# Performance work log

Measured on AMD Instinct MI355X. Metric: run time of the kernel, lower is better.

## Reference

```python
import jax, jax.numpy as jnp
import numpy as np

DIM_EMB = 1024
NUM_HEADS = 16
DIM_HEAD = DIM_EMB // NUM_HEADS  # 64


def setup_inputs() -> dict:
    key = jax.random.key(0)
    k1, k2, k3 = jax.random.split(key, 3)
    x = jax.random.normal(k1, (4, 2048, DIM_EMB), dtype=jnp.float32)
    # nn.Linear(dim_embedding, 3*h*d, bias=False): weight shape [out, in]
    w_qkv = jax.random.normal(k2, (3 * NUM_HEADS * DIM_HEAD, DIM_EMB), dtype=jnp.float32) * (DIM_EMB ** -0.5)
    w_out = jax.random.normal(k3, (DIM_EMB, NUM_HEADS * DIM_HEAD), dtype=jnp.float32) * ((NUM_HEADS * DIM_HEAD) ** -0.5)
    return {"x": x, "w_qkv": w_qkv, "w_out": w_out}


def reference(x, w_qkv, w_out):
    b, t, _ = x.shape
    scale = DIM_HEAD ** -0.5
    qkv = jnp.einsum('bte,fe->btf', x, w_qkv)  # [b, t, 3*h*d]
    qkv = qkv.reshape(b, t, 3, NUM_HEADS, DIM_HEAD)  # fused dim order (k h d)
    q, k, v = qkv[:, :, 0], qkv[:, :, 1], qkv[:, :, 2]  # each [b, t, h, d]
    scores = jnp.einsum('bihd,bjhd->bhij', q, k) * scale  # [b, h, t, t]
    weights = jax.nn.softmax(scores, axis=-1)
    attn = jnp.einsum('bhij,bjhd->bhid', weights, v)  # [b, h, t, d]
    concat = attn.transpose(0, 2, 1, 3).reshape(b, t, NUM_HEADS * DIM_HEAD)
    return jnp.einsum('btf,ef->bte', concat, w_out)
```

## Files before the change

### kernel.cpp

```cpp
#include <hip/hip_runtime.h>

#define DI __device__ __forceinline__

typedef float  f32x2  __attribute__((ext_vector_type(2)));
typedef float  f32x4  __attribute__((ext_vector_type(4)));
typedef float  f32x16 __attribute__((ext_vector_type(16)));
typedef __bf16 bf16x8 __attribute__((ext_vector_type(8)));
typedef unsigned u32x2 __attribute__((ext_vector_type(2)));
typedef unsigned u32x4 __attribute__((ext_vector_type(4)));

static constexpr int TB   = 2048;
static constexpr int NTOK = 8192;
static constexpr int EMB  = 1024;
static constexpr int FQKV = 3072;

DI unsigned short f2bf(float f) {
  union { float f; unsigned u; } v; v.f = f;
  unsigned r = v.u + 0x7FFFu + ((v.u >> 16) & 1u);
  return (unsigned short)(r >> 16);
}

DI unsigned pack2bf(float a, float b) {
#if __has_builtin(__builtin_amdgcn_cvt_pk_bf16_f32)
  typedef __bf16 bf16x2 __attribute__((ext_vector_type(2)));
  bf16x2 r = __builtin_amdgcn_cvt_pk_bf16_f32(a, b);
  return __builtin_bit_cast(unsigned, r);
#else
  unsigned ua = __builtin_bit_cast(unsigned, a) + 0x8000u;
  unsigned ub = __builtin_bit_cast(unsigned, b) + 0x8000u;
  return __builtin_amdgcn_perm(ub, ua, 0x07060302u);
#endif
}

DI void plswap(unsigned& a, unsigned& b) {
#if __has_builtin(__builtin_amdgcn_permlane32_swap)
  u32x2 r = __builtin_amdgcn_permlane32_swap(a, b, false, false);
  a = r.x; b = r.y;
#else
  const bool hi = (threadIdx.x & 32) != 0;
  unsigned ax = (unsigned)__shfl_xor((int)a, 32);
  unsigned bx = (unsigned)__shfl_xor((int)b, 32);
  unsigned na = hi ? bx : a;
  unsigned nb = hi ? b : ax;
  a = na; b = nb;
#endif
}

DI bf16x8 frag4(unsigned a, unsigned b, unsigned c, unsigned d) {
  u32x4 u = {a, b, c, d};
  return __builtin_bit_cast(bf16x8, u);
}

DI void gload16(const void* g, void* l) {
  __builtin_amdgcn_global_load_lds(
      (__attribute__((address_space(1))) void*)(g),
      (__attribute__((address_space(3))) void*)(l), 16, 0, 0);
}

DI void wait_vm8() { asm volatile("s_waitcnt vmcnt(8)" ::: "memory"); }
DI void wait_vm4() { asm volatile("s_waitcnt vmcnt(4)" ::: "memory"); }
DI void wait_vm0() { asm volatile("s_waitcnt vmcnt(0)" ::: "memory"); }
DI void rbar()     { __builtin_amdgcn_s_barrier(); }
DI void sfence()   { __builtin_amdgcn_sched_barrier(0); }

__global__ __launch_bounds__(256)
void cvt_kernel(const float4* __restrict__ x, const float4* __restrict__ wq,
                const float4* __restrict__ wo,
                ushort4* __restrict__ xb, ushort4* __restrict__ wqb,
                ushort4* __restrict__ wob) {
  const int i  = blockIdx.x * 256 + threadIdx.x;
  const int nx = NTOK * EMB / 4;
  const int nq = FQKV * EMB / 4;
  float4 v; ushort4* dst;
  if (i < nx)           { v = x[i];           dst = xb  + i; }
  else if (i < nx + nq) { v = wq[i - nx];     dst = wqb + (i - nx); }
  else                  { v = wo[i - nx - nq]; dst = wob + (i - nx - nq); }
  ushort4 p;
  p.x = f2bf(v.x); p.y = f2bf(v.y); p.z = f2bf(v.z); p.w = f2bf(v.w);
  *dst = p;
}

__global__ __launch_bounds__(512, 2)
void gemm256(const unsigned short* __restrict__ A,
             const unsigned short* __restrict__ Bt,
             const int K,
             unsigned short* __restrict__ qk,
             unsigned short* __restrict__ vT) {
  __shared__ unsigned short sA[2][256 * 64];
  __shared__ unsigned short sB[2][256 * 64];
  const int tid  = threadIdx.x;
  const int w    = tid >> 6;
  const int l    = tid & 63;
  const int quad = l >> 4;
  const int lr   = l & 15;
  const int nwg  = gridDim.x * gridDim.y;
  const int orig = blockIdx.y * gridDim.x + blockIdx.x;
  const int swz  = (orig & 7) * (nwg >> 3) + (orig >> 3);
  const int n0   = (swz % gridDim.x) * 256;
  const int m0   = (swz / gridDim.x) * 256;
  const int wm   = (w >> 2) * 128;
  const int wn   = (w & 3) * 64;

  f32x4 acc[8][4];
#pragma unroll
  for (int i = 0; i < 8; ++i)
#pragma unroll
    for (int j = 0; j < 4; ++j) acc[i][j] = {0.f, 0.f, 0.f, 0.f};

  const int srow8 = l >> 3;
  const int gsw   = ((l & 7) ^ srow8) * 8;
  const unsigned short* gA0 = A  + (long)(m0 + w * 8 + srow8) * K + gsw;
  const unsigned short* gB0 = Bt + (long)(n0 + w * 8 + srow8) * K + gsw;

  const int NT = K >> 6;

#define STAGE256(buf, kk)                                                      \
  do {                                                                         \
    _Pragma("unroll")                                                          \
    for (int jj = 0; jj < 4; ++jj) {                                           \
      gload16(gA0 + (long)jj * 64 * K + (kk), &sA[buf][(jj * 64 + w * 8) * 64]);\
      gload16(gB0 + (long)jj * 64 * K + (kk), &sB[buf][(jj * 64 + w * 8) * 64]);\
    }                                                                          \
  } while (0)

  STAGE256(0, 0);

  for (int t = 0; t < NT; ++t) {
    const int cur = t & 1;
    if (t + 1 < NT) { STAGE256(cur ^ 1, (t + 1) * 64); wait_vm8(); }
    else            { wait_vm0(); }
    sfence();
    rbar();
    sfence();
    const unsigned short* aS = &sA[cur][0];
    const unsigned short* bS = &sB[cur][0];
#pragma unroll
    for (int ks = 0; ks < 2; ++ks) {
      bf16x8 bfr[4];
#pragma unroll
      for (int nf = 0; nf < 4; ++nf) {
        const int r = wn + nf * 16 + lr;
        bfr[nf] = *(const bf16x8*)(bS + r * 64 + ((ks * 4 + quad) ^ (r & 7)) * 8);
      }
      __builtin_amdgcn_s_setprio(1);
#pragma unroll
      for (int m = 0; m < 8; ++m) {
        const int ra = wm + m * 16 + lr;
        const bf16x8 af = *(const bf16x8*)(aS + ra * 64 + ((ks * 4 + quad) ^ (ra & 7)) * 8);
#pragma unroll
        for (int nf = 0; nf < 4; ++nf)
          acc[m][nf] = __builtin_amdgcn_mfma_f32_16x16x32_bf16(af, bfr[nf],
                                                               acc[m][nf], 0, 0, 0);
      }
      __builtin_amdgcn_s_setprio(0);
    }
    sfence();
    rbar();
  }
#undef STAGE256

  if (n0 < 2048) {
    const float qs = (n0 < 1024) ? 0.18033688011112042f : 1.0f;
#pragma unroll
    for (int m = 0; m < 8; ++m) {
      const int row = m0 + wm + m * 16 + quad * 4;
#pragma unroll
      for (int nf = 0; nf < 4; ++nf) {
        const int col = n0 + wn + nf * 16 + lr;
#pragma unroll
        for (int r = 0; r < 4; ++r)
          qk[(long)(row + r) * 2048 + col] = f2bf(acc[m][nf][r] * qs);
      }
    }
  } else {
#pragma unroll
    for (int m = 0; m < 8; ++m) {
      const int tok = m0 + wm + m * 16 + quad * 4;
      const int bb  = tok >> 11, tt = tok & 2047;
#pragma unroll
      for (int nf = 0; nf < 4; ++nf) {
        const int fv = n0 - 2048 + wn + nf * 16 + lr;
        ushort4 p;
        p.x = f2bf(acc[m][nf][0]); p.y = f2bf(acc[m][nf][1]);
        p.z = f2bf(acc[m][nf][2]); p.w = f2bf(acc[m][nf][3]);
        *(ushort4*)(vT + ((long)(bb * 1024 + fv)) * 2048 + tt) = p;
      }
    }
  }
}

__global__ __launch_bounds__(256)
void gemm_out(const unsigned short* __restrict__ A,
              const unsigned short* __restrict__ Bt,
              const int K,
              float* __restrict__ outp) {
  __shared__ unsigned short sA[2][128 * 32];
  __shared__ unsigned short sB[2][128 * 32];
  const int tid  = threadIdx.x;
  const int w    = tid >> 6;
  const int l    = tid & 63;
  const int quad = l >> 4;
  const int lr   = l & 15;
  const int nwg  = gridDim.x * gridDim.y;
  const int orig = blockIdx.y * gridDim.x + blockIdx.x;
  const int swzb = (orig & 7) * (nwg >> 3) + (orig >> 3);
  const int n0   = (swzb % gridDim.x) * 128;
  const int m0   = (swzb / gridDim.x) * 128;
  const int wm   = (w >> 1) * 64;
  const int wn   = (w & 1) * 64;

  f32x4 acc[4][4];
#pragma unroll
  for (int i = 0; i < 4; ++i)
#pragma unroll
    for (int j = 0; j < 4; ++j) acc[i][j] = {0.f, 0.f, 0.f, 0.f};

  const int srow = l >> 2;
  const int sg   = (l & 3) ^ ((l >> 3) & 3);
  const unsigned short* gA = A  + (long)(m0 + w * 32 + srow) * K + sg * 8;
  const unsigned short* gB = Bt + (long)(n0 + w * 32 + srow) * K + sg * 8;
  const int lofs = w * 1024;
  const int swz  = (lr >> 1) & 3;
  const int NT   = K >> 5;

  gload16(gA,          &sA[0][lofs]);
  gload16(gA + 16 * K, &sA[0][lofs + 512]);
  gload16(gB,          &sB[0][lofs]);
  gload16(gB + 16 * K, &sB[0][lofs + 512]);

  for (int t = 0; t < NT; ++t) {
    const int cur = t & 1;
    if (t + 1 < NT) {
      const int k0 = (t + 1) * 32;
      gload16(gA + k0,          &sA[cur ^ 1][lofs]);
      gload16(gA + k0 + 16 * K, &sA[cur ^ 1][lofs + 512]);
      gload16(gB + k0,          &sB[cur ^ 1][lofs]);
      gload16(gB + k0 + 16 * K, &sB[cur ^ 1][lofs + 512]);
      wait_vm4();
    } else {
      wait_vm0();
    }
    sfence();
    rbar();
    sfence();
    bf16x8 af[4], bfr[4];
#pragma unroll
    for (int rt = 0; rt < 4; ++rt)
      af[rt] = *(const bf16x8*)(&sA[cur][(wm + rt * 16 + lr) * 32 + (quad ^ swz) * 8]);
#pragma unroll
    for (int ct = 0; ct < 4; ++ct)
      bfr[ct] = *(const bf16x8*)(&sB[cur][(wn + ct * 16 + lr) * 32 + (quad ^ swz) * 8]);
    __builtin_amdgcn_s_setprio(1);
#pragma unroll
    for (int rt = 0; rt < 4; ++rt)
#pragma unroll
      for (int ct = 0; ct < 4; ++ct)
        acc[rt][ct] = __builtin_amdgcn_mfma_f32_16x16x32_bf16(af[rt], bfr[ct],
                                                              acc[rt][ct], 0, 0, 0);
    __builtin_amdgcn_s_setprio(0);
    sfence();
    rbar();
  }

#pragma unroll
  for (int rt = 0; rt < 4; ++rt) {
    const int row = m0 + wm + rt * 16 + quad * 4;
#pragma unroll
    for (int ct = 0; ct < 4; ++ct) {
      const int col = n0 + wn + ct * 16 + lr;
#pragma unroll
      for (int r = 0; r < 4; ++r)
        outp[(long)(row + r) * 1024 + col] = acc[rt][ct][r];
    }
  }
}

__global__ __launch_bounds__(256, 4)
void attn_kernel(const unsigned short* __restrict__ qk,
                 const unsigned short* __restrict__ vT,
                 unsigned short* __restrict__ attnb) {
  __shared__ unsigned short sK[2][64 * 64];
  __shared__ unsigned short sV[2][64 * 64];
  const int tid = threadIdx.x;
  const int w   = tid >> 6;
  const int l   = tid & 63;
  const int l31 = l & 31;
  const int lh  = l >> 5;
  const int h8  = lh * 8;
  const int bh  = blockIdx.x;
  const int hh  = bh & 15;
  const long tokbase = (long)(bh >> 4) * TB;
  const int qbase = blockIdx.y * 128 + w * 32;

  bf16x8 qf[4];
  {
    const unsigned short* qptr = qk + (tokbase + qbase + l31) * 2048 + hh * 64 + h8;
#pragma unroll
    for (int s = 0; s < 4; ++s) qf[s] = *(const bf16x8*)(qptr + s * 16);
  }

  const int srow = l >> 3;
  const int g    = (l & 7) ^ srow;
  const unsigned short* kbase =
      qk + (tokbase + w * 16 + srow) * 2048 + 1024 + hh * 64 + g * 8;
  const unsigned short* vbase =
      vT + ((long)bh * 64 + w * 16 + srow) * 2048 + g * 8;

  f32x16 oacc[2] = {{}, {}};
  f32x2 lp2 = {0.f, 0.f};

  gload16(kbase,            &sK[0][(w * 16 + 0) * 64]);
  gload16(kbase + 8 * 2048, &sK[0][(w * 16 + 8) * 64]);
  gload16(vbase,            &sV[0][(w * 16 + 0) * 64]);
  gload16(vbase + 8 * 2048, &sV[0][(w * 16 + 8) * 64]);

  for (int t = 0; t < 32; ++t) {
    const int buf = t & 1;
    if (t + 1 < 32) {
      const int k0 = (t + 1) * 64;
      const int nb = buf ^ 1;
      gload16(kbase + (long)k0 * 2048,            &sK[nb][(w * 16 + 0) * 64]);
      gload16(kbase + (long)k0 * 2048 + 8 * 2048, &sK[nb][(w * 16 + 8) * 64]);
      gload16(vbase + k0,                         &sV[nb][(w * 16 + 0) * 64]);
      gload16(vbase + k0 + 8 * 2048,              &sV[nb][(w * 16 + 8) * 64]);
      wait_vm4();
    } else {
      wait_vm0();
    }
    sfence();
    rbar();
    sfence();
    const unsigned short* bK = sK[buf];
    const unsigned short* bV = sV[buf];

#pragma unroll
    for (int G = 0; G < 2; ++G) {
      f32x16 sacc = {};
      __builtin_amdgcn_s_setprio(1);
#pragma unroll
      for (int s = 0; s < 4; ++s) {
        const int key = G * 32 + l31;
        const int p   = (s * 2 + lh) ^ (key & 7);
        const bf16x8 kf = *(const bf16x8*)(bK + key * 64 + p * 8);
        sacc = __builtin_amdgcn_mfma_f32_32x32x16_bf16(kf, qf[s], sacc, 0, 0, 0);
      }
      __builtin_amdgcn_s_setprio(0);
      float e[16];
#pragma unroll
      for (int i = 0; i < 16; ++i) e[i] = __builtin_amdgcn_exp2f(sacc[i]);
#pragma unroll
      for (int i = 0; i < 8; ++i) {
        f32x2 pr = {e[2 * i], e[2 * i + 1]};
        lp2 += pr;
      }
      unsigned d[8];
#pragma unroll
      for (int i = 0; i < 8; ++i) d[i] = pack2bf(e[2 * i], e[2 * i + 1]);
      plswap(d[0], d[2]); plswap(d[1], d[3]);
      plswap(d[4], d[6]); plswap(d[5], d[7]);
      bf16x8 pp[2];
      pp[0] = frag4(d[0], d[1], d[2], d[3]);
      pp[1] = frag4(d[4], d[5], d[6], d[7]);
      __builtin_amdgcn_s_setprio(1);
#pragma unroll
      for (int sub = 0; sub < 2; ++sub) {
        const int gt  = (G * 2 + sub) * 2 + lh;
        const int d0r = l31, d1r = 32 + l31;
        const bf16x8 vf0 = *(const bf16x8*)(bV + d0r * 64 + ((gt ^ (d0r & 7))) * 8);
        const bf16x8 vf1 = *(const bf16x8*)(bV + d1r * 64 + ((gt ^ (d1r & 7))) * 8);
        oacc[0] = __builtin_amdgcn_mfma_f32_32x32x16_bf16(pp[sub], vf0, oacc[0], 0, 0, 0);
        oacc[1] = __builtin_amdgcn_mfma_f32_32x32x16_bf16(pp[sub], vf1, oacc[1], 0, 0, 0);
      }
      __builtin_amdgcn_s_setprio(0);
    }
    sfence();
    rbar();
  }

  const float lp = lp2.x + lp2.y;
  const float fs = lp + __shfl_xor(lp, 32);
  const float rc = 1.0f / fs;
#pragma unroll
  for (int r = 0; r < 16; ++r) {
    const int row = (r & 3) + 8 * (r >> 2) + 4 * lh;
    const float sc = __shfl(rc, row);
    const long base = (tokbase + qbase + row) * 1024 + hh * 64;
    attnb[base + l31]      = f2bf(oacc[0][r] * sc);
    attnb[base + 32 + l31] = f2bf(oacc[1][r] * sc);
  }
}

extern "C" void kernel_launch(void* const* d_in, const int* in_sizes, int n_in,
                              void* d_out, int out_size, void* d_ws, size_t ws_size,
                              hipStream_t stream) {
  const float* x    = (const float*)d_in[0];
  const float* wqkv = (const float*)d_in[1];
  const float* wout = (const float*)d_in[2];
  float* outp = (float*)d_out;

  unsigned short* xb    = (unsigned short*)d_ws;
  unsigned short* wqkvb = xb    + (long)NTOK * EMB;
  unsigned short* woutb = wqkvb + (long)FQKV * EMB;
  unsigned short* qkb   = woutb + (long)EMB * EMB;
  unsigned short* vTb   = qkb   + (long)NTOK * 2048;
  unsigned short* attnb = vTb   + (long)4 * 16 * 64 * TB;

  cvt_kernel<<<12288, 256, 0, stream>>>(
      (const float4*)x, (const float4*)wqkv, (const float4*)wout,
      (ushort4*)xb, (ushort4*)wqkvb, (ushort4*)woutb);

  gemm256<<<dim3(12, 32), 512, 0, stream>>>(xb, wqkvb, EMB, qkb, vTb);

  attn_kernel<<<dim3(64, 16), 256, 0, stream>>>(qkb, vTb, attnb);

  gemm_out<<<dim3(8, 64), 256, 0, stream>>>(attnb, woutb, EMB, outp);
}
```

Baseline: 277.1 us.

## Use 16-wave 256x256 GEMM tiles and split-K atomics for output projection

```diff
diff --git a/kernel.cpp b/kernel.cpp
--- a/kernel.cpp
+++ b/kernel.cpp
@@ -57,7 +57,6 @@
       (__attribute__((address_space(3))) void*)(l), 16, 0, 0);
 }
 
-DI void wait_vm8() { asm volatile("s_waitcnt vmcnt(8)" ::: "memory"); }
 DI void wait_vm4() { asm volatile("s_waitcnt vmcnt(4)" ::: "memory"); }
 DI void wait_vm0() { asm volatile("s_waitcnt vmcnt(0)" ::: "memory"); }
 DI void rbar()     { __builtin_amdgcn_s_barrier(); }
@@ -80,12 +79,14 @@
   *dst = p;
 }
 
-__global__ __launch_bounds__(512, 2)
-void gemm256(const unsigned short* __restrict__ A,
+template <int MODE>
+__global__ __launch_bounds__(1024)
+void gemm16w(const unsigned short* __restrict__ A,
              const unsigned short* __restrict__ Bt,
-             const int K,
+             const int Kstride, const int Klen,
              unsigned short* __restrict__ qk,
-             unsigned short* __restrict__ vT) {
+             unsigned short* __restrict__ vT,
+             float* __restrict__ outp) {
   __shared__ unsigned short sA[2][256 * 64];
   __shared__ unsigned short sB[2][256 * 64];
   const int tid  = threadIdx.x;
@@ -98,36 +99,37 @@
   const int swz  = (orig & 7) * (nwg >> 3) + (orig >> 3);
   const int n0   = (swz % gridDim.x) * 256;
   const int m0   = (swz / gridDim.x) * 256;
-  const int wm   = (w >> 2) * 128;
+  const int wm   = (w >> 2) * 64;
   const int wn   = (w & 3) * 64;
-
-  f32x4 acc[8][4];
-#pragma unroll
-  for (int i = 0; i < 8; ++i)
+  const int kofs = (MODE == 1) ? blockIdx.z * Klen : 0;
+
+  f32x4 acc[4][4];
+#pragma unroll
+  for (int i = 0; i < 4; ++i)
 #pragma unroll
     for (int j = 0; j < 4; ++j) acc[i][j] = {0.f, 0.f, 0.f, 0.f};
 
   const int srow8 = l >> 3;
   const int gsw   = ((l & 7) ^ srow8) * 8;
-  const unsigned short* gA0 = A  + (long)(m0 + w * 8 + srow8) * K + gsw;
-  const unsigned short* gB0 = Bt + (long)(n0 + w * 8 + srow8) * K + gsw;
-
-  const int NT = K >> 6;
-
-#define STAGE256(buf, kk)                                                      \
+  const unsigned short* gA0 = A  + (long)(m0 + w * 16 + srow8) * Kstride + kofs + gsw;
+  const unsigned short* gB0 = Bt + (long)(n0 + w * 16 + srow8) * Kstride + kofs + gsw;
+
+  const int NT = Klen >> 6;
+
+#define STAGE16(buf, kk)                                                       \
   do {                                                                         \
     _Pragma("unroll")                                                          \
-    for (int jj = 0; jj < 4; ++jj) {                                           \
-      gload16(gA0 + (long)jj * 64 * K + (kk), &sA[buf][(jj * 64 + w * 8) * 64]);\
-      gload16(gB0 + (long)jj * 64 * K + (kk), &sB[buf][(jj * 64 + w * 8) * 64]);\
+    for (int jj = 0; jj < 2; ++jj) {                                           \
+      gload16(gA0 + (long)jj * 8 * Kstride + (kk), &sA[buf][(w * 16 + jj * 8) * 64]); \
+      gload16(gB0 + (long)jj * 8 * Kstride + (kk), &sB[buf][(w * 16 + jj * 8) * 64]); \
     }                                                                          \
   } while (0)
 
-  STAGE256(0, 0);
+  STAGE16(0, 0);
 
   for (int t = 0; t < NT; ++t) {
     const int cur = t & 1;
-    if (t + 1 < NT) { STAGE256(cur ^ 1, (t + 1) * 64); wait_vm8(); }
+    if (t + 1 < NT) { STAGE16(cur ^ 1, (t + 1) * 64); wait_vm4(); }
     else            { wait_vm0(); }
     sfence();
     rbar();
@@ -140,13 +142,13 @@
 #pragma unroll
       for (int nf = 0; nf < 4; ++nf) {
         const int r = wn + nf * 16 + lr;
-        bfr[nf] = *(const bf16x8*)(bS + r * 64 + ((ks * 4 + quad) ^ (r & 7)) * 8);
+        bfr[nf] = *(const bf16x8*)(bS + r * 64 + (((ks * 4 + quad) ^ (r & 7)) * 8));
       }
       __builtin_amdgcn_s_setprio(1);
 #pragma unroll
-      for (int m = 0; m < 8; ++m) {
+      for (int m = 0; m < 4; ++m) {
         const int ra = wm + m * 16 + lr;
-        const bf16x8 af = *(const bf16x8*)(aS + ra * 64 + ((ks * 4 + quad) ^ (ra & 7)) * 8);
+        const bf16x8 af = *(const bf16x8*)(aS + ra * 64 + (((ks * 4 + quad) ^ (ra & 7)) * 8));
 #pragma unroll
         for (int nf = 0; nf < 4; ++nf)
           acc[m][nf] = __builtin_amdgcn_mfma_f32_16x16x32_bf16(af, bfr[nf],
@@ -157,120 +159,48 @@
     sfence();
     rbar();
   }
-#undef STAGE256
-
-  if (n0 < 2048) {
-    const float qs = (n0 < 1024) ? 0.18033688011112042f : 1.0f;
-#pragma unroll
-    for (int m = 0; m < 8; ++m) {
+#undef STAGE16
+
+  if (MODE == 0) {
+    if (n0 < 2048) {
+      const float qs = (n0 < 1024) ? 0.18033688011112042f : 1.0f;
+#pragma unroll
+      for (int m = 0; m < 4; ++m) {
+        const int row = m0 + wm + m * 16 + quad * 4;
+#pragma unroll
+        for (int nf = 0; nf < 4; ++nf) {
+          const int col = n0 + wn + nf * 16 + lr;
+#pragma unroll
+          for (int r = 0; r < 4; ++r)
+            qk[(long)(row + r) * 2048 + col] = f2bf(acc[m][nf][r] * qs);
+        }
+      }
+    } else {
+#pragma unroll
+      for (int m = 0; m < 4; ++m) {
+        const int tok = m0 + wm + m * 16 + quad * 4;
+        const int bb  = tok >> 11, tt = tok & 2047;
+#pragma unroll
+        for (int nf = 0; nf < 4; ++nf) {
+          const int fv = n0 - 2048 + wn + nf * 16 + lr;
+          ushort4 p;
+          p.x = f2bf(acc[m][nf][0]); p.y = f2bf(acc[m][nf][1]);
+          p.z = f2bf(acc[m][nf][2]); p.w = f2bf(acc[m][nf][3]);
+          *(ushort4*)(vT + ((long)(bb * 1024 + fv)) * 2048 + tt) = p;
+        }
+      }
+    }
+  } else {
+#pragma unroll
+    for (int m = 0; m < 4; ++m) {
       const int row = m0 + wm + m * 16 + quad * 4;
 #pragma unroll
       for (int nf = 0; nf < 4; ++nf) {
         const int col = n0 + wn + nf * 16 + lr;
 #pragma unroll
         for (int r = 0; r < 4; ++r)
-          qk[(long)(row + r) * 2048 + col] = f2bf(acc[m][nf][r] * qs);
-      }
-    }
-  } else {
-#pragma unroll
-    for (int m = 0; m < 8; ++m) {
-      const int tok = m0 + wm + m * 16 + quad * 4;
-      const int bb  = tok >> 11, tt = tok & 2047;
-#pragma unroll
-      for (int nf = 0; nf < 4; ++nf) {
-        const int fv = n0 - 2048 + wn + nf * 16 + lr;
-        ushort4 p;
-        p.x = f2bf(acc[m][nf][0]); p.y = f2bf(acc[m][nf][1]);
-        p.z = f2bf(acc[m][nf][2]); p.w = f2bf(acc[m][nf][3]);
-        *(ushort4*)(vT + ((long)(bb * 1024 + fv)) * 2048 + tt) = p;
-      }
-    }
-  }
-}
-
-__global__ __launch_bounds__(256)
-void gemm_out(const unsigned short* __restrict__ A,
-              const unsigned short* __restrict__ Bt,
-              const int K,
-              float* __restrict__ outp) {
-  __shared__ unsigned short sA[2][128 * 32];
-  __shared__ unsigned short sB[2][128 * 32];
-  const int tid  = threadIdx.x;
-  const int w    = tid >> 6;
-  const int l    = tid & 63;
-  const int quad = l >> 4;
-  const int lr   = l & 15;
-  const int nwg  = gridDim.x * gridDim.y;
-  const int orig = blockIdx.y * gridDim.x + blockIdx.x;
-  const int swzb = (orig & 7) * (nwg >> 3) + (orig >> 3);
-  const int n0   = (swzb % gridDim.x) * 128;
-  const int m0   = (swzb / gridDim.x) * 128;
-  const int wm   = (w >> 1) * 64;
-  const int wn   = (w & 1) * 64;
-
-  f32x4 acc[4][4];
-#pragma unroll
-  for (int i = 0; i < 4; ++i)
-#pragma unroll
-    for (int j = 0; j < 4; ++j) acc[i][j] = {0.f, 0.f, 0.f, 0.f};
-
-  const int srow = l >> 2;
-  const int sg   = (l & 3) ^ ((l >> 3) & 3);
-  const unsigned short* gA = A  + (long)(m0 + w * 32 + srow) * K + sg * 8;
-  const unsigned short* gB = Bt + (long)(n0 + w * 32 + srow) * K + sg * 8;
-  const int lofs = w * 1024;
-  const int swz  = (lr >> 1) & 3;
-  const int NT   = K >> 5;
-
-  gload16(gA,          &sA[0][lofs]);
-  gload16(gA + 16 * K, &sA[0][lofs + 512]);
-  gload16(gB,          &sB[0][lofs]);
-  gload16(gB + 16 * K, &sB[0][lofs + 512]);
-
-  for (int t = 0; t < NT; ++t) {
-    const int cur = t & 1;
-    if (t + 1 < NT) {
-      const int k0 = (t + 1) * 32;
-      gload16(gA + k0,          &sA[cur ^ 1][lofs]);
-      gload16(gA + k0 + 16 * K, &sA[cur ^ 1][lofs + 512]);
-      gload16(gB + k0,          &sB[cur ^ 1][lofs]);
-      gload16(gB + k0 + 16 * K, &sB[cur ^ 1][lofs + 512]);
-      wait_vm4();
-    } else {
-      wait_vm0();
-    }
-    sfence();
-    rbar();
-    sfence();
-    bf16x8 af[4], bfr[4];
-#pragma unroll
-    for (int rt = 0; rt < 4; ++rt)
-      af[rt] = *(const bf16x8*)(&sA[cur][(wm + rt * 16 + lr) * 32 + (quad ^ swz) * 8]);
-#pragma unroll
-    for (int ct = 0; ct < 4; ++ct)
-      bfr[ct] = *(const bf16x8*)(&sB[cur][(wn + ct * 16 + lr) * 32 + (quad ^ swz) * 8]);
-    __builtin_amdgcn_s_setprio(1);
-#pragma unroll
-    for (int rt = 0; rt < 4; ++rt)
-#pragma unroll
-      for (int ct = 0; ct < 4; ++ct)
-        acc[rt][ct] = __builtin_amdgcn_mfma_f32_16x16x32_bf16(af[rt], bfr[ct],
-                                                              acc[rt][ct], 0, 0, 0);
-    __builtin_amdgcn_s_setprio(0);
-    sfence();
-    rbar();
-  }
-
-#pragma unroll
-  for (int rt = 0; rt < 4; ++rt) {
-    const int row = m0 + wm + rt * 16 + quad * 4;
-#pragma unroll
-    for (int ct = 0; ct < 4; ++ct) {
-      const int col = n0 + wn + ct * 16 + lr;
-#pragma unroll
-      for (int r = 0; r < 4; ++r)
-        outp[(long)(row + r) * 1024 + col] = acc[rt][ct][r];
+          atomicAdd(&outp[(long)(row + r) * 1024 + col], acc[m][nf][r]);
+      }
     }
   }
 }
@@ -409,9 +339,12 @@
       (const float4*)x, (const float4*)wqkv, (const float4*)wout,
       (ushort4*)xb, (ushort4*)wqkvb, (ushort4*)woutb);
 
-  gemm256<<<dim3(12, 32), 512, 0, stream>>>(xb, wqkvb, EMB, qkb, vTb);
+  gemm16w<0><<<dim3(12, 32), 1024, 0, stream>>>(
+      xb, wqkvb, EMB, EMB, qkb, vTb, nullptr);
 
   attn_kernel<<<dim3(64, 16), 256, 0, stream>>>(qkb, vTb, attnb);
 
-  gemm_out<<<dim3(8, 64), 256, 0, stream>>>(attnb, woutb, EMB, outp);
-}
+  hipMemsetAsync(outp, 0, (size_t)NTOK * EMB * sizeof(float), stream);
+  gemm16w<1><<<dim3(4, 32, 2), 1024, 0, stream>>>(
+      attnb, woutb, EMB, 512, nullptr, nullptr, outp);
+}
```

After: 319.4 us. +15.3%, slower.
